# Kernel optimization log

Measured on AMD Instinct MI355X. Metric: run time of the kernel, lower is better.

## Reference

```python
import jax, jax.numpy as jnp
import numpy as np

D_MODEL = 1024
HEAD_SIZE = 128
SCALE = float(np.sqrt(HEAD_SIZE))


def setup_inputs() -> dict:
    key = jax.random.key(0)
    kx, kq, kk, kv = jax.random.split(key, 4)
    B, T = 4, 4096
    x = jax.random.normal(kx, (B, T, D_MODEL), dtype=jnp.float32)
    # torch nn.Linear(d_model, head_size, bias=False) weight: [head_size, d_model]
    s = 1.0 / np.sqrt(D_MODEL)
    Wq = jax.random.uniform(kq, (HEAD_SIZE, D_MODEL), jnp.float32, -s, s)
    Wk = jax.random.uniform(kk, (HEAD_SIZE, D_MODEL), jnp.float32, -s, s)
    Wv = jax.random.uniform(kv, (HEAD_SIZE, D_MODEL), jnp.float32, -s, s)
    return {"x": x, "Wq": Wq, "Wk": Wk, "Wv": Wv}


def reference(x, Wq, Wk, Wv):
    B, T, C = x.shape
    q = jnp.einsum('btc,hc->bth', x, Wq)  # [B,T,hs]
    k = jnp.einsum('btc,hc->bth', x, Wk)
    v = jnp.einsum('btc,hc->bth', x, Wv)
    scores = jnp.einsum('bth,bsh->bts', q, k) / SCALE  # [B,T,T]
    causal = jnp.tril(jnp.ones((T, T), dtype=bool))
    scores = jnp.where(causal, scores, -jnp.inf)
    attn = jax.nn.softmax(scores, axis=-1)
    # dropout p=0.0 -> identity
    return jnp.einsum('bts,bsh->bth', attn, v)
```

## Files before the change

### kernel.cpp

```cpp
#include <hip/hip_runtime.h>


typedef __attribute__((ext_vector_type(8))) short short8;
typedef __attribute__((ext_vector_type(8))) unsigned short ushort8;
typedef __attribute__((ext_vector_type(4))) unsigned short ushort4v;
typedef __attribute__((ext_vector_type(4))) float f32x4;
typedef __attribute__((ext_vector_type(16))) float f32x16;
typedef __attribute__((ext_vector_type(4))) int int4v;
typedef __attribute__((ext_vector_type(2))) unsigned int u32x2;
typedef unsigned int u32;
typedef unsigned short u16;

#define MFMA32(a, b, c) __builtin_amdgcn_mfma_f32_32x32x16_bf16((a), (b), (c), 0, 0, 0)
#define WAITVM0() asm volatile("s_waitcnt vmcnt(0)" ::: "memory")
#define NEG_INF (-1e30f)

#define CHUNK 10
#define PITEMS 119
#define NITEMS 476

__device__ __forceinline__ void gload16(const void* g, void* l) {
  __builtin_amdgcn_global_load_lds((const __attribute__((address_space(1))) u32*)g,
                                   (__attribute__((address_space(3))) u32*)l, 16, 0, 0);
}

__device__ __forceinline__ u16 f2bf(float f) {
  u32 u = __builtin_bit_cast(u32, f);
  u = u + 0x7FFFu + ((u >> 16) & 1u);
  return (u16)(u >> 16);
}

__device__ __forceinline__ u32 cvtpk(float lo, float hi) {
  u32 r;
  asm("v_cvt_pk_bf16_f32 %0, %1, %2" : "=v"(r) : "v"(lo), "v"(hi));
  return r;
}

__global__ __launch_bounds__(256) void wconv_kernel(const float* __restrict__ Wq,
                                                    const float* __restrict__ Wk,
                                                    const float* __restrict__ Wv,
                                                    u16* __restrict__ Wb) {
  int g = (blockIdx.x * 256 + threadIdx.x) * 8;
  const float* src;
  if (g < 131072)      src = Wq + g;
  else if (g < 262144) src = Wk + (g - 131072);
  else                 src = Wv + (g - 262144);
  float4 a = *(const float4*)src;
  float4 b = *(const float4*)(src + 4);
  ushort8 o;
  o[0] = f2bf(a.x); o[1] = f2bf(a.y); o[2] = f2bf(a.z); o[3] = f2bf(a.w);
  o[4] = f2bf(b.x); o[5] = f2bf(b.y); o[6] = f2bf(b.z); o[7] = f2bf(b.w);
  *(ushort8*)(Wb + g) = o;
}

#define QK_SCALE 0.127517446f

__global__ __launch_bounds__(256, 2) void qkv_proj_kernel(const float* __restrict__ x,
                                                          const u16* __restrict__ Wb,
                                                          u16* __restrict__ qout,
                                                          u16* __restrict__ kout,
                                                          u16* __restrict__ vtout) {
  __shared__ __align__(16) unsigned char Wlds[2][24576];
  __shared__ __align__(16) unsigned char Xlds[2][8192];
  const int tid = threadIdx.x;
  const int w = tid >> 6;
  const int l = tid & 63;
  const int h = l >> 5, n32 = l & 31;
  const int mh = w >> 1, ng = w & 1;
  const int bx = (int)blockIdx.x;
  const int ns = bx >> 8;
  const int m0 = (bx & 255) * 64;

  const int xr = tid >> 2, xc = tid & 3;
  const float* xsrc = x + (size_t)(m0 + xr) * 1024 + xc * 16;
  const int xsw = (xr & 7) << 4;
  unsigned char* const xw[2] = {
    (unsigned char*)Xlds[0] + xr * 128,
    (unsigned char*)Xlds[1] + xr * 128};

  f32x16 acc[3];
#pragma unroll
  for (int j = 0; j < 3; ++j)
#pragma unroll
    for (int r = 0; r < 16; ++r) acc[j][r] = 0.f;

#define STAGE_W(buf, ks)                                                       \
  {                                                                            \
    _Pragma("unroll") for (int c = 0; c < 6; ++c) {                            \
      int L = c * 256 + tid;                                                   \
      int row = L >> 3, chp = L & 7;                                           \
      int gch = chp ^ (row & 7);                                               \
      gload16((const char*)Wb + (size_t)(ns * 192 + row) * 2048 + (ks) * 128 + \
                  gch * 16,                                                    \
              (unsigned char*)Wlds[buf] + c * 4096 + w * 1024);                \
    }                                                                          \
  }
#define WRITE_X(buf)                                                           \
  {                                                                            \
    int4v p0, p1;                                                              \
    p0[0] = (int)cvtpk(xa0.x, xa0.y); p0[1] = (int)cvtpk(xa0.z, xa0.w);        \
    p0[2] = (int)cvtpk(xa1.x, xa1.y); p0[3] = (int)cvtpk(xa1.z, xa1.w);        \
    p1[0] = (int)cvtpk(xa2.x, xa2.y); p1[1] = (int)cvtpk(xa2.z, xa2.w);        \
    p1[2] = (int)cvtpk(xa3.x, xa3.y); p1[3] = (int)cvtpk(xa3.z, xa3.w);        \
    *(int4v*)(xw[buf] + ((xc * 32) ^ xsw)) = p0;                               \
    *(int4v*)(xw[buf] + ((xc * 32 + 16) ^ xsw)) = p1;                          \
  }

  float4 xa0 = *(const float4*)(xsrc);
  float4 xa1 = *(const float4*)(xsrc + 4);
  float4 xa2 = *(const float4*)(xsrc + 8);
  float4 xa3 = *(const float4*)(xsrc + 12);
  STAGE_W(0, 0);

  const int am = mh * 32 + n32;
  const int asw = (am & 7) << 4;
  int cur = 0;

  for (int ks = 0; ks < 16; ++ks) {
    WRITE_X(cur);
    __syncthreads();
    if (ks < 15) {
      xa0 = *(const float4*)(xsrc + (ks + 1) * 64);
      xa1 = *(const float4*)(xsrc + (ks + 1) * 64 + 4);
      xa2 = *(const float4*)(xsrc + (ks + 1) * 64 + 8);
      xa3 = *(const float4*)(xsrc + (ks + 1) * 64 + 12);
      STAGE_W(cur ^ 1, ks + 1);
    }
    const char* xb0 = (const char*)Xlds[cur];
    const char* wb0 = (const char*)Wlds[cur];
    __builtin_amdgcn_s_setprio(1);
#pragma unroll
    for (int k16 = 0; k16 < 4; ++k16) {
      short8 a = *(const short8*)(xb0 + am * 128 + ((k16 * 32 + h * 16) ^ asw));
#pragma unroll
      for (int j = 0; j < 3; ++j) {
        int nrow = (ng * 3 + j) * 32 + n32;
        short8 b = *(const short8*)(wb0 + nrow * 128 +
                                    ((k16 * 32 + h * 16) ^ ((nrow & 7) << 4)));
        acc[j] = MFMA32(a, b, acc[j]);
      }
    }
    __builtin_amdgcn_s_setprio(0);
    cur ^= 1;
  }
#undef STAGE_W
#undef WRITE_X

  const int m0e = m0 + mh * 32;
#pragma unroll
  for (int j = 0; j < 3; ++j) {
    int tig = ns * 6 + ng * 3 + j;
    int gcol = tig * 32 + n32;
    if (tig < 4) {
#pragma unroll
      for (int r = 0; r < 16; ++r) {
        int row = m0e + (r & 3) + 8 * (r >> 2) + 4 * h;
        qout[(size_t)row * 128 + gcol] = f2bf(acc[j][r] * QK_SCALE);
      }
    } else if (tig < 8) {
#pragma unroll
      for (int r = 0; r < 16; ++r) {
        int row = m0e + (r & 3) + 8 * (r >> 2) + 4 * h;
        kout[(size_t)row * 128 + (gcol - 128)] = f2bf(acc[j][r]);
      }
    } else {
      int d = gcol - 256;
#pragma unroll
      for (int rq = 0; rq < 4; ++rq) {
        int t0 = m0e + rq * 8 + 4 * h;
        ushort4v o4;
#pragma unroll
        for (int i = 0; i < 4; ++i) o4[i] = f2bf(acc[j][rq * 4 + i]);
        *(ushort4v*)&vtout[(size_t)((t0 >> 12) * 128 + d) * 4096 + (t0 & 4095)] = o4;
      }
    }
  }
}

template <bool SPLIT>
__global__ __launch_bounds__(256, 2) void attn_kernel(const u16* __restrict__ qws,
                                                      const u16* __restrict__ kws,
                                                      const u16* __restrict__ vtws,
                                                      float* __restrict__ out,
                                                      float* __restrict__ opart,
                                                      float* __restrict__ mlpart) {
  __shared__ __align__(16) unsigned char Klds[2][16384];
  __shared__ __align__(16) unsigned char Vlds[2][16384];

  const int tid = threadIdx.x;
  const int w = tid >> 6;
  const int l = tid & 63;
  const int h = l >> 5, q32 = l & 31;

  int bi, qt, s_lo, s_hi, item;
  if constexpr (SPLIT) {
    item = (int)blockIdx.x;
    bi = item / PITEMS;
    int r = item - bi * PITEMS;
    int base = 0;
    qt = 0;
    while (true) {
      int cnt = (qt + 5) / 5;
      if (r < base + cnt) { break; }
      base += cnt;
      ++qt;
    }
    int cc = r - base;
    int nsteps = 2 * qt + 2;
    s_lo = cc * CHUNK;
    s_hi = (s_lo + CHUNK < nsteps) ? s_lo + CHUNK : nsteps;
  } else {
    item = 0;
    int tb = (int)blockIdx.x;
    bi = tb & 3;
    qt = 31 - (tb >> 2);
    s_lo = 0;
    s_hi = 2 * qt + 2;
  }

  const int q0w = qt * 128 + w * 32;
  const int qg = q0w + q32;
  const int grow = bi * 4096 + qg;
  const int ql = w * 32 + q32;

  short8 qf[8];
  const u16* qp = qws + (size_t)grow * 128 + h * 8;
#pragma unroll
  for (int ks = 0; ks < 8; ++ks) qf[ks] = *(const short8*)(qp + ks * 16);

  f32x16 ot[4];
#pragma unroll
  for (int dt = 0; dt < 4; ++dt)
#pragma unroll
    for (int r = 0; r < 16; ++r) ot[dt][r] = 0.f;
  float mreg = NEG_INF, lsum = 0.f;

  const char* kbatch = (const char*)kws + (size_t)bi * 4096 * 256;
  const char* vbatch = (const char*)vtws + (size_t)bi * 128 * 8192;

#define STAGE_KV(buf, kv0)                                                     \
  {                                                                            \
    _Pragma("unroll") for (int c = 0; c < 4; ++c) {                            \
      int L = c * 256 + tid;                                                   \
      int row = L >> 4, chp = L & 15;                                          \
      int gch = chp ^ (row & 7);                                               \
      gload16(kbatch + (size_t)((kv0) + row) * 256 + gch * 16,                 \
              (unsigned char*)Klds[buf] + c * 4096 + w * 1024);                \
    }                                                                          \
    _Pragma("unroll") for (int c = 0; c < 4; ++c) {                            \
      int L = c * 256 + tid;                                                   \
      int row = L >> 3, chp = L & 7;                                           \
      int gch = chp ^ (row & 7);                                               \
      gload16(vbatch + (size_t)row * 8192 + (size_t)(kv0) * 2 + gch * 16,      \
              (unsigned char*)Vlds[buf] + c * 4096 + w * 1024);                \
    }                                                                          \
  }

  STAGE_KV(0, s_lo * 64);
  int cur = 0;

  for (int s = s_lo; s < s_hi; ++s) {
    WAITVM0();
    __builtin_amdgcn_s_barrier();
    __builtin_amdgcn_sched_barrier(0);
    if (s + 1 < s_hi) STAGE_KV(cur ^ 1, (s + 1) * 64);
    const int kv0 = s * 64;
    const bool active = (kv0 <= q0w + 31);

    if (active) {
      f32x16 st0, st1;
#pragma unroll
      for (int r = 0; r < 16; ++r) { st0[r] = 0.f; st1[r] = 0.f; }
      const char* Kb = (const char*)Klds[cur];
      const int sw = (q32 & 7) << 4;
      __builtin_amdgcn_s_setprio(1);
#pragma unroll
      for (int ks = 0; ks < 8; ++ks) {
        int coff = ks * 32 + h * 16;
        short8 a0 = *(const short8*)(Kb + q32 * 256 + (coff ^ sw));
        st0 = MFMA32(a0, qf[ks], st0);
        short8 a1 = *(const short8*)(Kb + (32 + q32) * 256 + (coff ^ sw));
        st1 = MFMA32(a1, qf[ks], st1);
      }
      __builtin_amdgcn_s_setprio(0);

      if (kv0 + 63 > q0w) {
#pragma unroll
        for (int r = 0; r < 16; ++r) {
          int kvr = kv0 + (r & 3) + 8 * (r >> 2) + 4 * h;
          if (kvr > qg) st0[r] = NEG_INF;
          if (kvr + 32 > qg) st1[r] = NEG_INF;
        }
      }

      float tmax = st0[0];
#pragma unroll
      for (int r = 1; r < 16; ++r) tmax = fmaxf(tmax, st0[r]);
#pragma unroll
      for (int r = 0; r < 16; ++r) tmax = fmaxf(tmax, st1[r]);
      tmax = fmaxf(tmax, __shfl_xor(tmax, 32));
      if (!__all(tmax <= mreg + 8.0f)) {
        float mnew = fmaxf(mreg, tmax);
        float alpha = exp2f(mreg - mnew);
        lsum *= alpha;
#pragma unroll
        for (int dt = 0; dt < 4; ++dt)
#pragma unroll
          for (int r = 0; r < 16; ++r) ot[dt][r] *= alpha;
        mreg = mnew;
      }
      float rs = 0.f;
#pragma unroll
      for (int r = 0; r < 16; ++r) { st0[r] = exp2f(st0[r] - mreg); rs += st0[r]; }
#pragma unroll
      for (int r = 0; r < 16; ++r) { st1[r] = exp2f(st1[r] - mreg); rs += st1[r]; }
      rs += __shfl_xor(rs, 32);
      lsum += rs;

      const char* Vb = (const char*)Vlds[cur];
      __builtin_amdgcn_s_setprio(1);
#pragma unroll
      for (int t = 0; t < 4; ++t) {
        const f32x16& stt = (t < 2) ? st0 : st1;
        const int rb = (t & 1) * 8;
        u32 A0 = cvtpk(stt[rb + 0], stt[rb + 1]);
        u32 C0 = cvtpk(stt[rb + 2], stt[rb + 3]);
        u32 B0 = cvtpk(stt[rb + 4], stt[rb + 5]);
        u32 D0 = cvtpk(stt[rb + 6], stt[rb + 7]);
        u32 Ax = (u32)__shfl_xor((int)A0, 32);
        u32 Bx = (u32)__shfl_xor((int)B0, 32);
        u32 Cx = (u32)__shfl_xor((int)C0, 32);
        u32 Dx = (u32)__shfl_xor((int)D0, 32);
        int4v pbv;
        pbv[0] = (int)(h ? Bx : A0);
        pbv[1] = (int)(h ? Dx : C0);
        pbv[2] = (int)(h ? B0 : Ax);
        pbv[3] = (int)(h ? D0 : Cx);
        short8 pb = __builtin_bit_cast(short8, pbv);
#pragma unroll
        for (int dt = 0; dt < 4; ++dt) {
          int row = dt * 32 + q32;
          short8 va = *(const short8*)(Vb + row * 128 + ((t * 32 + h * 16) ^ sw));
          ot[dt] = MFMA32(va, pb, ot[dt]);
        }
      }
      __builtin_amdgcn_s_setprio(0);
    }
    cur ^= 1;
  }

  if constexpr (!SPLIT) {
    float inv = 1.0f / lsum;
    float* ob = out + (size_t)grow * 128;
#pragma unroll
    for (int dt = 0; dt < 4; ++dt)
#pragma unroll
      for (int rq = 0; rq < 4; ++rq) {
        f32x4 v4;
#pragma unroll
        for (int i = 0; i < 4; ++i) v4[i] = ot[dt][rq * 4 + i] * inv;
        *(f32x4*)(ob + dt * 32 + rq * 8 + 4 * h) = v4;
      }
  } else {
    float* ob = opart + (size_t)item * 16384 + (size_t)ql * 128;
#pragma unroll
    for (int dt = 0; dt < 4; ++dt)
#pragma unroll
      for (int rq = 0; rq < 4; ++rq) {
        f32x4 v4;
#pragma unroll
        for (int i = 0; i < 4; ++i) v4[i] = ot[dt][rq * 4 + i];
        *(f32x4*)(ob + dt * 32 + rq * 8 + 4 * h) = v4;
      }
    if (h == 0) {
      mlpart[item * 128 + ql] = mreg;
      mlpart[NITEMS * 128 + item * 128 + ql] = lsum;
    }
  }
#undef STAGE_KV
}

__global__ __launch_bounds__(256) void combine_kernel(const float* __restrict__ opart,
                                                      const float* __restrict__ mlpart,
                                                      float* __restrict__ out) {
  int idx = blockIdx.x * 256 + threadIdx.x;
  int row = idx >> 7, d = idx & 127;
  int bi = row >> 12, lrow = row & 4095;
  int qt = lrow >> 7, ql = lrow & 127;
  int base = 0;
#pragma unroll 1
  for (int j = 0; j < qt; ++j) base += (j + 5) / 5;
  int nspl = (qt + 5) / 5;
  int it0 = bi * PITEMS + base;

  float M = NEG_INF;
#pragma unroll 1
  for (int j = 0; j < nspl; ++j)
    M = fmaxf(M, mlpart[(it0 + j) * 128 + ql]);
  float L = 0.f, O = 0.f;
#pragma unroll 1
  for (int j = 0; j < nspl; ++j) {
    float s = exp2f(mlpart[(it0 + j) * 128 + ql] - M);
    L += mlpart[NITEMS * 128 + (it0 + j) * 128 + ql] * s;
    O += opart[(size_t)(it0 + j) * 16384 + (size_t)ql * 128 + d] * s;
  }
  out[(size_t)row * 128 + d] = O / L;
}

extern "C" void kernel_launch(void* const* d_in, const int* in_sizes, int n_in,
                              void* d_out, int out_size, void* d_ws, size_t ws_size,
                              hipStream_t stream) {
  (void)in_sizes; (void)n_in; (void)out_size;
  const float* x  = (const float*)d_in[0];
  const float* Wq = (const float*)d_in[1];
  const float* Wk = (const float*)d_in[2];
  const float* Wv = (const float*)d_in[3];
  float* out = (float*)d_out;
  char* ws = (char*)d_ws;
  u16* qws  = (u16*)(ws);
  u16* kws  = (u16*)(ws + (4u << 20));
  u16* vtws = (u16*)(ws + (8u << 20));
  u16* Wb   = (u16*)(ws + (12u << 20));
  float* opart  = (float*)(ws + (13u << 20));
  float* mlpart = (float*)(ws + (47u << 20));

  wconv_kernel<<<dim3(192), dim3(256), 0, stream>>>(Wq, Wk, Wv, Wb);
  qkv_proj_kernel<<<dim3(512), dim3(256), 0, stream>>>(x, Wb, qws, kws, vtws);
  if (ws_size >= ((size_t)48 << 20)) {
    attn_kernel<true><<<dim3(NITEMS), dim3(256), 0, stream>>>(qws, kws, vtws, nullptr, opart, mlpart);
    combine_kernel<<<dim3(8192), dim3(256), 0, stream>>>(opart, mlpart, out);
  } else {
    attn_kernel<false><<<dim3(128), dim3(256), 0, stream>>>(qws, kws, vtws, out, nullptr, nullptr);
  }
}
```

Before: 91.02 us.

## Register-stage QKV projection loads with two-deep prefetch and interleave block mapping

The QKV projection kernel stops using direct global-to-LDS loads for the weights. It now loads both x and W tiles into registers two k-steps ahead, in alternating A/B register sets, then writes them to double-buffered LDS between raw barriers guarded by sched_barrier. The block index mapping also changes so that the two column halves (ns) of the same 64-row tile are adjacent blocks, which should improve L2 reuse of x. The deeper prefetch is meant to hide global latency, but it raises register pressure and adds VGPR-to-LDS write traffic for W.

```diff
diff --git a/kernel.cpp b/kernel.cpp
--- a/kernel.cpp
+++ b/kernel.cpp
@@ -7,12 +7,13 @@
 typedef __attribute__((ext_vector_type(4))) float f32x4;
 typedef __attribute__((ext_vector_type(16))) float f32x16;
 typedef __attribute__((ext_vector_type(4))) int int4v;
-typedef __attribute__((ext_vector_type(2))) unsigned int u32x2;
 typedef unsigned int u32;
 typedef unsigned short u16;
 
 #define MFMA32(a, b, c) __builtin_amdgcn_mfma_f32_32x32x16_bf16((a), (b), (c), 0, 0, 0)
 #define WAITVM0() asm volatile("s_waitcnt vmcnt(0)" ::: "memory")
+#define WAITLGKM0() asm volatile("s_waitcnt lgkmcnt(0)" ::: "memory")
+#define SCHEDB() __builtin_amdgcn_sched_barrier(0)
 #define NEG_INF (-1e30f)
 
 #define CHUNK 10
@@ -66,17 +67,25 @@
   const int w = tid >> 6;
   const int l = tid & 63;
   const int h = l >> 5, n32 = l & 31;
-  const int mh = w >> 1, ng = w & 1;
+  const int wm = w >> 1, wn = w & 1;
   const int bx = (int)blockIdx.x;
-  const int ns = bx >> 8;
-  const int m0 = (bx & 255) * 64;
+  const int ns = bx & 1;
+  const int m0 = (bx >> 1) * 64;
 
   const int xr = tid >> 2, xc = tid & 3;
   const float* xsrc = x + (size_t)(m0 + xr) * 1024 + xc * 16;
   const int xsw = (xr & 7) << 4;
-  unsigned char* const xw[2] = {
-    (unsigned char*)Xlds[0] + xr * 128,
-    (unsigned char*)Xlds[1] + xr * 128};
+  const int xo0 = xr * 128 + ((xc * 32) ^ xsw);
+  const int xo1 = xr * 128 + ((xc * 32 + 16) ^ xsw);
+  const u16* wg[6];
+  int wo[6];
+#pragma unroll
+  for (int c = 0; c < 6; ++c) {
+    int L = c * 256 + tid;
+    int row = L >> 3, chp = L & 7;
+    wg[c] = Wb + (size_t)(ns * 192 + row) * 1024 + chp * 8;
+    wo[c] = row * 128 + ((chp * 16) ^ ((row & 7) << 4));
+  }
 
   f32x16 acc[3];
 #pragma unroll
@@ -84,72 +93,105 @@
 #pragma unroll
     for (int r = 0; r < 16; ++r) acc[j][r] = 0.f;
 
-#define STAGE_W(buf, ks)                                                       \
+#define LOADS(S, k)                                                            \
+  x##S##0 = *(const float4*)(xsrc + (k) * 64);                                 \
+  x##S##1 = *(const float4*)(xsrc + (k) * 64 + 4);                             \
+  x##S##2 = *(const float4*)(xsrc + (k) * 64 + 8);                             \
+  x##S##3 = *(const float4*)(xsrc + (k) * 64 + 12);                            \
+  w##S##0 = *(const ushort8*)(wg[0] + (k) * 64);                               \
+  w##S##1 = *(const ushort8*)(wg[1] + (k) * 64);                               \
+  w##S##2 = *(const ushort8*)(wg[2] + (k) * 64);                               \
+  w##S##3 = *(const ushort8*)(wg[3] + (k) * 64);                               \
+  w##S##4 = *(const ushort8*)(wg[4] + (k) * 64);                               \
+  w##S##5 = *(const ushort8*)(wg[5] + (k) * 64);
+
+#define WRITES(S, buf)                                                         \
   {                                                                            \
-    _Pragma("unroll") for (int c = 0; c < 6; ++c) {                            \
-      int L = c * 256 + tid;                                                   \
-      int row = L >> 3, chp = L & 7;                                           \
-      int gch = chp ^ (row & 7);                                               \
-      gload16((const char*)Wb + (size_t)(ns * 192 + row) * 2048 + (ks) * 128 + \
-                  gch * 16,                                                    \
-              (unsigned char*)Wlds[buf] + c * 4096 + w * 1024);                \
+    float4 t0 = x##S##0;                                                       \
+    float4 t1 = x##S##1;                                                       \
+    float4 t2 = x##S##2;                                                       \
+    float4 t3 = x##S##3;                                                       \
+    ushort8 u0 = w##S##0;                                                      \
+    ushort8 u1 = w##S##1;                                                      \
+    ushort8 u2 = w##S##2;                                                      \
+    ushort8 u3 = w##S##3;                                                      \
+    ushort8 u4 = w##S##4;                                                      \
+    ushort8 u5 = w##S##5;                                                      \
+    int4v p0, p1;                                                              \
+    p0[0] = (int)cvtpk(t0.x, t0.y);                                            \
+    p0[1] = (int)cvtpk(t0.z, t0.w);                                            \
+    p0[2] = (int)cvtpk(t1.x, t1.y);                                            \
+    p0[3] = (int)cvtpk(t1.z, t1.w);                                            \
+    p1[0] = (int)cvtpk(t2.x, t2.y);                                            \
+    p1[1] = (int)cvtpk(t2.z, t2.w);                                            \
+    p1[2] = (int)cvtpk(t3.x, t3.y);                                            \
+    p1[3] = (int)cvtpk(t3.z, t3.w);                                            \
+    *(int4v*)((unsigned char*)Xlds[buf] + xo0) = p0;                           \
+    *(int4v*)((unsigned char*)Xlds[buf] + xo1) = p1;                           \
+    *(ushort8*)((unsigned char*)Wlds[buf] + wo[0]) = u0;                       \
+    *(ushort8*)((unsigned char*)Wlds[buf] + wo[1]) = u1;                       \
+    *(ushort8*)((unsigned char*)Wlds[buf] + wo[2]) = u2;                       \
+    *(ushort8*)((unsigned char*)Wlds[buf] + wo[3]) = u3;                       \
+    *(ushort8*)((unsigned char*)Wlds[buf] + wo[4]) = u4;                       \
+    *(ushort8*)((unsigned char*)Wlds[buf] + wo[5]) = u5;                       \
+  }
+
+#define COMPUTE(buf)                                                           \
+  {                                                                            \
+    const char* xb0 = (const char*)Xlds[buf];                                  \
+    const char* wb0 = (const char*)Wlds[buf];                                  \
+    __builtin_amdgcn_s_setprio(1);                                             \
+    _Pragma("unroll") for (int k16 = 0; k16 < 4; ++k16) {                      \
+      short8 a = *(const short8*)(xb0 + am * 128 +                             \
+                                  ((k16 * 32 + h * 16) ^ asw));                \
+      _Pragma("unroll") for (int j = 0; j < 3; ++j) {                          \
+        int nrow = (wn * 3 + j) * 32 + n32;                                    \
+        short8 b = *(const short8*)(wb0 + nrow * 128 +                         \
+                                    ((k16 * 32 + h * 16) ^ ((nrow & 7) << 4)));\
+        acc[j] = MFMA32(a, b, acc[j]);                                         \
+      }                                                                        \
     }                                                                          \
-  }
-#define WRITE_X(buf)                                                           \
-  {                                                                            \
-    int4v p0, p1;                                                              \
-    p0[0] = (int)cvtpk(xa0.x, xa0.y); p0[1] = (int)cvtpk(xa0.z, xa0.w);        \
-    p0[2] = (int)cvtpk(xa1.x, xa1.y); p0[3] = (int)cvtpk(xa1.z, xa1.w);        \
-    p1[0] = (int)cvtpk(xa2.x, xa2.y); p1[1] = (int)cvtpk(xa2.z, xa2.w);        \
-    p1[2] = (int)cvtpk(xa3.x, xa3.y); p1[3] = (int)cvtpk(xa3.z, xa3.w);        \
-    *(int4v*)(xw[buf] + ((xc * 32) ^ xsw)) = p0;                               \
-    *(int4v*)(xw[buf] + ((xc * 32 + 16) ^ xsw)) = p1;                          \
-  }
-
-  float4 xa0 = *(const float4*)(xsrc);
-  float4 xa1 = *(const float4*)(xsrc + 4);
-  float4 xa2 = *(const float4*)(xsrc + 8);
-  float4 xa3 = *(const float4*)(xsrc + 12);
-  STAGE_W(0, 0);
-
-  const int am = mh * 32 + n32;
+    __builtin_amdgcn_s_setprio(0);                                             \
+  }
+
+  const int am = wm * 32 + n32;
   const int asw = (am & 7) << 4;
-  int cur = 0;
-
-  for (int ks = 0; ks < 16; ++ks) {
-    WRITE_X(cur);
-    __syncthreads();
-    if (ks < 15) {
-      xa0 = *(const float4*)(xsrc + (ks + 1) * 64);
-      xa1 = *(const float4*)(xsrc + (ks + 1) * 64 + 4);
-      xa2 = *(const float4*)(xsrc + (ks + 1) * 64 + 8);
-      xa3 = *(const float4*)(xsrc + (ks + 1) * 64 + 12);
-      STAGE_W(cur ^ 1, ks + 1);
-    }
-    const char* xb0 = (const char*)Xlds[cur];
-    const char* wb0 = (const char*)Wlds[cur];
-    __builtin_amdgcn_s_setprio(1);
-#pragma unroll
-    for (int k16 = 0; k16 < 4; ++k16) {
-      short8 a = *(const short8*)(xb0 + am * 128 + ((k16 * 32 + h * 16) ^ asw));
-#pragma unroll
-      for (int j = 0; j < 3; ++j) {
-        int nrow = (ng * 3 + j) * 32 + n32;
-        short8 b = *(const short8*)(wb0 + nrow * 128 +
-                                    ((k16 * 32 + h * 16) ^ ((nrow & 7) << 4)));
-        acc[j] = MFMA32(a, b, acc[j]);
-      }
-    }
-    __builtin_amdgcn_s_setprio(0);
-    cur ^= 1;
-  }
-#undef STAGE_W
-#undef WRITE_X
-
-  const int m0e = m0 + mh * 32;
+
+  float4 xA0, xA1, xA2, xA3, xB0, xB1, xB2, xB3;
+  ushort8 wA0, wA1, wA2, wA3, wA4, wA5, wB0, wB1, wB2, wB3, wB4, wB5;
+
+  LOADS(A, 0);
+  LOADS(B, 1);
+  WRITES(A, 0);
+  LOADS(A, 2);
+  SCHEDB();
+
+  for (int s = 0; s < 16; s += 2) {
+    WAITLGKM0();
+    SCHEDB();
+    __builtin_amdgcn_s_barrier();
+    SCHEDB();
+    WRITES(B, 1);
+    if (s + 3 < 16) { LOADS(B, s + 3); }
+    SCHEDB();
+    COMPUTE(0);
+    WAITLGKM0();
+    SCHEDB();
+    __builtin_amdgcn_s_barrier();
+    SCHEDB();
+    if (s + 2 < 16) { WRITES(A, 0); }
+    if (s + 4 < 16) { LOADS(A, s + 4); }
+    SCHEDB();
+    COMPUTE(1);
+  }
+#undef LOADS
+#undef WRITES
+#undef COMPUTE
+
+  const int m0e = m0 + wm * 32;
 #pragma unroll
   for (int j = 0; j < 3; ++j) {
-    int tig = ns * 6 + ng * 3 + j;
+    int tig = ns * 6 + wn * 3 + j;
     int gcol = tig * 32 + n32;
     if (tig < 4) {
 #pragma unroll
```

Result: slower. 94.24 us (+3.5%).
